# Kernel optimization log

Hardware: AMD Instinct MI355X
Metric: run time of the kernel (lower is better)

Reference implementation:

```python
import jax, jax.numpy as jnp
import numpy as np


def setup_inputs() -> dict:
    key = jax.random.key(0)
    k1, k2, k3 = jax.random.split(key, 3)
    B, S, D = 4, 2048, 1024   # batch, seq_len, hidden
    M = 65536                 # external memory size
    x = jax.random.normal(k1, (B, S, D), dtype=jnp.float32)
    keys = jax.random.normal(k2, (M, D), dtype=jnp.float32)
    vals = jax.random.normal(k3, (M, D), dtype=jnp.float32)
    return {"x": x, "ver": 1, "keys": keys, "vals": vals}


def reference(x, ver, keys, vals):
    # linear_attention: unnormalized attention over external memory.
    #   out = (x @ keys^T) @ vals
    # Use associativity to avoid materializing the [B,S,M] score matrix:
    #   kv = keys^T @ vals  -> [D, D]
    kv = jnp.einsum("md,me->de", keys, vals)   # [D, D]
    out = jnp.einsum("bsd,de->bse", x, kv)      # [B, S, D]
    return out
```

## Files before the change

kernel.cpp:

```cpp
#include <hip/hip_runtime.h>
#include <hip/hip_bf16.h>


typedef __attribute__((ext_vector_type(8))) __bf16 bf16x8;
typedef __attribute__((ext_vector_type(4))) __bf16 bf16x4;
typedef __attribute__((ext_vector_type(4))) float  f32x4;

#define D_DIM   1024
#define M_DIM   65536
#define ROWS    8192
#define NCHUNK  16
#define MC      (M_DIM / NCHUNK)
#define BT      128
#define BK      64
#define LDK     72
#define TILE_BYTES 16384

__device__ __forceinline__ f32x4 mfma16(bf16x8 a, bf16x8 b, f32x4 c) {
    return __builtin_amdgcn_mfma_f32_16x16x32_bf16(a, b, c, 0, 0, 0);
}

__device__ __forceinline__ void gl_lds16(const void* gsrc, void* ldst) {
    __builtin_amdgcn_global_load_lds(
        (const __attribute__((address_space(1))) unsigned int*)gsrc,
        (__attribute__((address_space(3))) unsigned int*)ldst,
        16, 0, 0);
}

__global__ __launch_bounds__(512)
void convert_tile(const float* __restrict__ keys,
                  const float* __restrict__ vals,
                  __hip_bfloat16* __restrict__ KtT,
                  __hip_bfloat16* __restrict__ VtT)
{
    __shared__ __align__(16) char Lt[1024 * 128];

    const float* src = blockIdx.z ? vals : keys;
    char* dstb = (char*)(blockIdx.z ? VtT : KtT);

    const int tid = threadIdx.x;
    const int s   = blockIdx.x;
    const int m0  = s * 64;

    const int dc = tid & 255;
    const int qh = tid >> 8;
    #pragma unroll
    for (int i = 0; i < 8; ++i) {
        const int q = 2 * i + qh;
        f32x4 v[4];
        #pragma unroll
        for (int r = 0; r < 4; ++r)
            v[r] = *(const f32x4*)(src + (size_t)(m0 + 4 * q + r) * D_DIM + 4 * dc);
        const int p8 = q ^ (dc & 15);
        #pragma unroll
        for (int j = 0; j < 4; ++j) {
            bf16x4 w;
            #pragma unroll
            for (int r = 0; r < 4; ++r) w[r] = (__bf16)v[r][j];
            *(bf16x4*)(Lt + (4 * dc + j) * 128 + p8 * 8) = w;
        }
    }
    __syncthreads();

    #pragma unroll
    for (int ii = 0; ii < 16; ++ii) {
        const int idx = tid + ii * 512;
        const int t   = idx >> 10;
        const int dl  = (idx >> 3) & 127;
        const int c   = idx & 7;
        const int d   = t * 128 + dl;
        const int cl  = c ^ (dl & 7);
        const int h   = (dl >> 2) & 15;
        const int g0  = (2 * cl)     ^ h;
        const int g1  = (2 * cl + 1) ^ h;
        bf16x4 lo = *(const bf16x4*)(Lt + d * 128 + g0 * 8);
        bf16x4 hi = *(const bf16x4*)(Lt + d * 128 + g1 * 8);
        bf16x8 w;
        w[0] = lo[0]; w[1] = lo[1]; w[2] = lo[2]; w[3] = lo[3];
        w[4] = hi[0]; w[5] = hi[1]; w[6] = hi[2]; w[7] = hi[3];
        char* dst_tile = dstb + ((size_t)t * 1024 + s) * TILE_BYTES;
        *(bf16x8*)(dst_tile + dl * 128 + c * 16) = w;
    }
}

__global__ __launch_bounds__(512, 2)
void kv_gemm8(const __hip_bfloat16* __restrict__ VtT,
              const __hip_bfloat16* __restrict__ KtT,
              float* __restrict__ kvw)
{
    __shared__ __align__(16) char lds[2][4][TILE_BYTES];

    const int tid  = threadIdx.x;
    const int lane = tid & 63;
    const int wave = tid >> 6;
    const int we   = wave >> 2;
    const int wd   = wave & 3;

    const int bx    = blockIdx.x;
    const int xcd   = bx & 7;
    const int idx   = bx >> 3;
    const int chunk = ((idx >> 4) << 3) | xcd;
    const int t16   = idx & 15;
    const int E8    = t16 >> 2;
    const int D8    = t16 & 3;

    const size_t step0 = (size_t)chunk * 64;

    const char* Vb = (const char*)VtT;
    const char* Kb = (const char*)KtT;

    const int l15 = lane & 15;
    const int l7  = lane & 7;
    const int hi  = lane >> 4;

    f32x4 acc[8][4] = {};

    auto tileptr = [&](const char* base, int rt, int t) -> const char* {
        return base + ((size_t)rt * 1024 + step0 + (size_t)t) * TILE_BYTES;
    };
    auto stage_sub = [&](int buf, int sub, const char* tile) {
        char* dst = &lds[buf][sub][wave * 1024];
        const char* s = tile + wave * 1024 + lane * 16;
        gl_lds16(s,        dst);
        gl_lds16(s + 8192, dst + 8192);
    };

    stage_sub(0, 0, tileptr(Vb, 2 * E8,     0));
    stage_sub(0, 1, tileptr(Vb, 2 * E8 + 1, 0));
    stage_sub(0, 2, tileptr(Kb, 2 * D8,     0));
    stage_sub(0, 3, tileptr(Kb, 2 * D8 + 1, 0));
    asm volatile("s_waitcnt vmcnt(0)" ::: "memory");
    __builtin_amdgcn_s_barrier();

    bf16x8 bfr[4][2];

    #pragma unroll 2
    for (int t = 0; t < 64; ++t) {
        const int buf = t & 1;
        const char* abase = &lds[buf][we][0];
        const char* bbase = &lds[buf][2 + (wd >> 1)][0];
        const int brow0 = (wd & 1) * 64;

        #pragma unroll
        for (int p = 0; p < 4; ++p) {
            bf16x8 afr[2][2];
            #pragma unroll
            for (int j = 0; j < 2; ++j)
                #pragma unroll
                for (int ks = 0; ks < 2; ++ks) {
                    const int row = (2 * p + j) * 16 + l15;
                    afr[j][ks] = *(const bf16x8*)(abase + row * 128
                                   + (((ks << 2) + hi) ^ l7) * 16);
                }
            if (p == 0) {
                #pragma unroll
                for (int n = 0; n < 4; ++n)
                    #pragma unroll
                    for (int ks = 0; ks < 2; ++ks) {
                        const int row = brow0 + n * 16 + l15;
                        bfr[n][ks] = *(const bf16x8*)(bbase + row * 128
                                       + (((ks << 2) + hi) ^ l7) * 16);
                    }
            }
            if (p == 0 && t + 1 < 64) {
                stage_sub(buf ^ 1, 0, tileptr(Vb, 2 * E8,     t + 1));
                stage_sub(buf ^ 1, 1, tileptr(Vb, 2 * E8 + 1, t + 1));
            }
            if (p == 1 && t + 1 < 64) {
                stage_sub(buf ^ 1, 2, tileptr(Kb, 2 * D8,     t + 1));
                stage_sub(buf ^ 1, 3, tileptr(Kb, 2 * D8 + 1, t + 1));
            }
            __builtin_amdgcn_s_barrier();
            asm volatile("s_waitcnt lgkmcnt(0)" ::: "memory");
            __builtin_amdgcn_sched_barrier(0);
            __builtin_amdgcn_s_setprio(1);
            #pragma unroll
            for (int j = 0; j < 2; ++j)
                #pragma unroll
                for (int n = 0; n < 4; ++n)
                    #pragma unroll
                    for (int ks = 0; ks < 2; ++ks)
                        acc[2 * p + j][n] = mfma16(afr[j][ks], bfr[n][ks],
                                                   acc[2 * p + j][n]);
            __builtin_amdgcn_s_setprio(0);
            if (p == 3)
                asm volatile("s_waitcnt vmcnt(0)" ::: "memory");
            __builtin_amdgcn_s_barrier();
        }
    }

    const int rb = hi * 4;
    #pragma unroll
    for (int mi = 0; mi < 8; ++mi) {
        #pragma unroll
        for (int ni = 0; ni < 4; ++ni) {
            const int d = D8 * 256 + wd * 64 + ni * 16 + l15;
            #pragma unroll
            for (int r = 0; r < 4; ++r) {
                const int e = E8 * 256 + we * 128 + mi * 16 + rb + r;
                atomicAdd(kvw + (size_t)e * D_DIM + d, acc[mi][ni][r]);
            }
        }
    }
}

__global__ __launch_bounds__(256)
void kv_partial_kernel(const float* __restrict__ keys,
                       const float* __restrict__ vals,
                       float* __restrict__ kvw)
{
    __shared__ __bf16 Ktl[BT][LDK];
    __shared__ __bf16 Vtl[BT][LDK];

    const int tid  = threadIdx.x;
    const int lane = tid & 63;
    const int wave = tid >> 6;
    const int wr   = wave >> 1;
    const int wc   = wave & 1;

    const int tile  = blockIdx.x & 63;
    const int chunk = blockIdx.x >> 6;
    const int d0 = (tile >> 3) * BT;
    const int e0 = (tile & 7) * BT;
    const size_t mbeg = (size_t)chunk * MC;

    f32x4 acc[4][4] = {};
    const int kg  = tid & 15;
    const int d4a = tid >> 4;

    for (int ms = 0; ms < MC; ms += BK) {
        #pragma unroll
        for (int i = 0; i < 2; ++i) {
            const int dloc = (d4a + i * 16) * 4;
            const size_t mrow = mbeg + ms + (size_t)kg * 4;
            f32x4 kr[4], vr[4];
            #pragma unroll
            for (int r = 0; r < 4; ++r) {
                kr[r] = *(const f32x4*)(keys + (mrow + r) * D_DIM + d0 + dloc);
                vr[r] = *(const f32x4*)(vals + (mrow + r) * D_DIM + e0 + dloc);
            }
            #pragma unroll
            for (int j = 0; j < 4; ++j) {
                bf16x4 wk, wv;
                #pragma unroll
                for (int r = 0; r < 4; ++r) {
                    wk[r] = (__bf16)kr[r][j];
                    wv[r] = (__bf16)vr[r][j];
                }
                *(bf16x4*)&Ktl[dloc + j][kg * 4] = wk;
                *(bf16x4*)&Vtl[dloc + j][kg * 4] = wv;
            }
        }
        __syncthreads();

        #pragma unroll
        for (int ks = 0; ks < BK; ks += 32) {
            bf16x8 af[4], bf[4];
            #pragma unroll
            for (int t = 0; t < 4; ++t) {
                af[t] = *(const bf16x8*)&Ktl[wr * 64 + t * 16 + (lane & 15)][ks + (lane >> 4) * 8];
                bf[t] = *(const bf16x8*)&Vtl[wc * 64 + t * 16 + (lane & 15)][ks + (lane >> 4) * 8];
            }
            #pragma unroll
            for (int mi = 0; mi < 4; ++mi)
                #pragma unroll
                for (int ni = 0; ni < 4; ++ni)
                    acc[mi][ni] = mfma16(af[mi], bf[ni], acc[mi][ni]);
        }
        __syncthreads();
    }

    const int rbase = (lane >> 4) * 4;
    const int cidx  = lane & 15;
    #pragma unroll
    for (int mi = 0; mi < 4; ++mi) {
        #pragma unroll
        for (int ni = 0; ni < 4; ++ni) {
            const int e = e0 + wc * 64 + ni * 16 + cidx;
            #pragma unroll
            for (int reg = 0; reg < 4; ++reg) {
                const int d = d0 + wr * 64 + mi * 16 + rbase + reg;
                atomicAdd(kvw + (size_t)e * D_DIM + d, acc[mi][ni][reg]);
            }
        }
    }
}

__global__ __launch_bounds__(256)
void out_gemm_kernel(const float* __restrict__ x,
                     const float* __restrict__ kvw,
                     float* __restrict__ out)
{
    __shared__ __bf16 Xt[BT][LDK];
    __shared__ __bf16 Wt[BT][LDK];

    const int tid  = threadIdx.x;
    const int lane = tid & 63;
    const int wave = tid >> 6;
    const int wr   = wave >> 1;
    const int wc   = wave & 1;

    const int r0 = blockIdx.x * BT;
    const int e0 = blockIdx.y * BT;

    f32x4 acc[4][4] = {};

    for (int ks0 = 0; ks0 < D_DIM; ks0 += BK) {
        #pragma unroll
        for (int i = 0; i < 8; ++i) {
            const int idx = tid + i * 256;
            const int row = idx >> 4;
            const int col = (idx & 15) * 4;
            f32x4 xa = *(const f32x4*)(x   + (size_t)(r0 + row) * D_DIM + ks0 + col);
            f32x4 wa = *(const f32x4*)(kvw + (size_t)(e0 + row) * D_DIM + ks0 + col);
            bf16x4 xb, wb;
            #pragma unroll
            for (int j = 0; j < 4; ++j) {
                xb[j] = (__bf16)xa[j];
                wb[j] = (__bf16)wa[j];
            }
            *(bf16x4*)&Xt[row][col] = xb;
            *(bf16x4*)&Wt[row][col] = wb;
        }
        __syncthreads();

        #pragma unroll
        for (int ks = 0; ks < BK; ks += 32) {
            bf16x8 af[4], bf[4];
            #pragma unroll
            for (int t = 0; t < 4; ++t) {
                af[t] = *(const bf16x8*)&Xt[wr * 64 + t * 16 + (lane & 15)][ks + (lane >> 4) * 8];
                bf[t] = *(const bf16x8*)&Wt[wc * 64 + t * 16 + (lane & 15)][ks + (lane >> 4) * 8];
            }
            #pragma unroll
            for (int mi = 0; mi < 4; ++mi)
                #pragma unroll
                for (int ni = 0; ni < 4; ++ni)
                    acc[mi][ni] = mfma16(af[mi], bf[ni], acc[mi][ni]);
        }
        __syncthreads();
    }

    const int rbase = (lane >> 4) * 4;
    const int cidx  = lane & 15;
    #pragma unroll
    for (int mi = 0; mi < 4; ++mi) {
        #pragma unroll
        for (int ni = 0; ni < 4; ++ni) {
            const int e = e0 + wc * 64 + ni * 16 + cidx;
            #pragma unroll
            for (int reg = 0; reg < 4; ++reg) {
                const int r = r0 + wr * 64 + mi * 16 + rbase + reg;
                out[(size_t)r * D_DIM + e] = acc[mi][ni][reg];
            }
        }
    }
}

extern "C" void kernel_launch(void* const* d_in, const int* in_sizes, int n_in,
                              void* d_out, int out_size, void* d_ws, size_t ws_size,
                              hipStream_t stream) {
    const float* x    = (const float*)d_in[0];
    const float* keys = (const float*)d_in[2];
    const float* vals = (const float*)d_in[3];
    float* out = (float*)d_out;

    const size_t kvw_bytes = (size_t)D_DIM * D_DIM * sizeof(float);
    const size_t kt_bytes  = (size_t)D_DIM * M_DIM * sizeof(__hip_bfloat16);
    const size_t need      = kvw_bytes + 2 * kt_bytes;

    float* kvw = (float*)d_ws;
    hipMemsetAsync(kvw, 0, kvw_bytes, stream);

    if (ws_size >= need) {
        __hip_bfloat16* KtT = (__hip_bfloat16*)((char*)d_ws + kvw_bytes);
        __hip_bfloat16* VtT = (__hip_bfloat16*)((char*)d_ws + kvw_bytes + kt_bytes);
        convert_tile<<<dim3(M_DIM / 64, 1, 2), dim3(512), 0, stream>>>(
            keys, vals, KtT, VtT);
        kv_gemm8<<<dim3(256), dim3(512), 0, stream>>>(VtT, KtT, kvw);
    } else {
        kv_partial_kernel<<<dim3(64 * NCHUNK), dim3(256), 0, stream>>>(keys, vals, kvw);
    }
    out_gemm_kernel<<<dim3(64, 8), dim3(256), 0, stream>>>(x, kvw, out);
}
```

Measured before the change: 353.9 us.

## Pre-convert x and kv to swizzled bf16 tiles for MFMA output GEMM

Adds a convert_rows kernel that turns x and the fp32 kv matrix into swizzled bf16 tiles. It also adds an out_gemm8 kernel that runs the output GEMM with bf16 MFMA, direct global-to-LDS loads and double buffering, in place of the old out_gemm_kernel. Separately, convert_tile is split along the D dimension so each block uses half the LDS, which doubles the grid and should raise occupancy. The new path needs extra workspace for the bf16 copies and falls back to the old kernel when the workspace is too small. The extra conversion passes add memory traffic and launch overhead, and rounding x and kv to bf16 reduces precision of the output.

```diff
diff --git a/kernel.cpp b/kernel.cpp
--- a/kernel.cpp
+++ b/kernel.cpp
@@ -33,24 +33,26 @@
                   __hip_bfloat16* __restrict__ KtT,
                   __hip_bfloat16* __restrict__ VtT)
 {
-    __shared__ __align__(16) char Lt[1024 * 128];
+    __shared__ __align__(16) char Lt[512 * 128];
 
     const float* src = blockIdx.z ? vals : keys;
     char* dstb = (char*)(blockIdx.z ? VtT : KtT);
 
-    const int tid = threadIdx.x;
-    const int s   = blockIdx.x;
-    const int m0  = s * 64;
-
-    const int dc = tid & 255;
-    const int qh = tid >> 8;
-    #pragma unroll
-    for (int i = 0; i < 8; ++i) {
-        const int q = 2 * i + qh;
+    const int tid  = threadIdx.x;
+    const int s    = blockIdx.x;
+    const int half = blockIdx.y;
+    const int m0   = s * 64;
+    const int d0   = half * 512;
+
+    const int dc = tid & 127;
+    const int qh = tid >> 7;
+    #pragma unroll
+    for (int i = 0; i < 4; ++i) {
+        const int q = 4 * i + qh;
         f32x4 v[4];
         #pragma unroll
         for (int r = 0; r < 4; ++r)
-            v[r] = *(const f32x4*)(src + (size_t)(m0 + 4 * q + r) * D_DIM + 4 * dc);
+            v[r] = *(const f32x4*)(src + (size_t)(m0 + 4 * q + r) * D_DIM + d0 + 4 * dc);
         const int p8 = q ^ (dc & 15);
         #pragma unroll
         for (int j = 0; j < 4; ++j) {
@@ -63,7 +65,7 @@
     __syncthreads();
 
     #pragma unroll
-    for (int ii = 0; ii < 16; ++ii) {
+    for (int ii = 0; ii < 8; ++ii) {
         const int idx = tid + ii * 512;
         const int t   = idx >> 10;
         const int dl  = (idx >> 3) & 127;
@@ -74,12 +76,36 @@
         const int g0  = (2 * cl)     ^ h;
         const int g1  = (2 * cl + 1) ^ h;
         bf16x4 lo = *(const bf16x4*)(Lt + d * 128 + g0 * 8);
-        bf16x4 hi = *(const bf16x4*)(Lt + d * 128 + g1 * 8);
+        bf16x4 hv = *(const bf16x4*)(Lt + d * 128 + g1 * 8);
         bf16x8 w;
         w[0] = lo[0]; w[1] = lo[1]; w[2] = lo[2]; w[3] = lo[3];
-        w[4] = hi[0]; w[5] = hi[1]; w[6] = hi[2]; w[7] = hi[3];
-        char* dst_tile = dstb + ((size_t)t * 1024 + s) * TILE_BYTES;
+        w[4] = hv[0]; w[5] = hv[1]; w[6] = hv[2]; w[7] = hv[3];
+        char* dst_tile = dstb + ((size_t)(half * 4 + t) * 1024 + s) * TILE_BYTES;
         *(bf16x8*)(dst_tile + dl * 128 + c * 16) = w;
+    }
+}
+
+__global__ __launch_bounds__(256)
+void convert_rows(const float* __restrict__ src,
+                  __hip_bfloat16* __restrict__ dstT)
+{
+    const int tid = threadIdx.x;
+    const int rt  = blockIdx.x;
+    const int t   = blockIdx.y;
+    const int r0  = rt * 128, d0 = t * 64;
+    char* tile = (char*)dstT + ((size_t)rt * 16 + t) * TILE_BYTES;
+    #pragma unroll
+    for (int it = 0; it < 4; ++it) {
+        const int idx = tid + it * 256;
+        const int r   = idx >> 3;
+        const int cl  = idx & 7;
+        const float* p = src + (size_t)(r0 + r) * D_DIM + d0 + cl * 8;
+        f32x4 a = *(const f32x4*)p;
+        f32x4 b = *(const f32x4*)(p + 4);
+        bf16x8 w;
+        w[0] = (__bf16)a[0]; w[1] = (__bf16)a[1]; w[2] = (__bf16)a[2]; w[3] = (__bf16)a[3];
+        w[4] = (__bf16)b[0]; w[5] = (__bf16)b[1]; w[6] = (__bf16)b[2]; w[7] = (__bf16)b[3];
+        *(bf16x8*)(tile + r * 128 + ((cl ^ (r & 7)) * 16)) = w;
     }
 }
 
@@ -204,6 +230,114 @@
     }
 }
 
+__global__ __launch_bounds__(512, 1)
+void out_gemm8(const __hip_bfloat16* __restrict__ xbT,
+               const __hip_bfloat16* __restrict__ kvbT,
+               float* __restrict__ out)
+{
+    __shared__ __align__(16) char lds[2][3][TILE_BYTES];
+
+    const int tid  = threadIdx.x;
+    const int lane = tid & 63;
+    const int wave = tid >> 6;
+    const int wr   = wave >> 2;
+    const int wee  = wave & 3;
+
+    const int bx = blockIdx.x;
+    const int rt = bx & 63;
+    const int be = bx >> 6;
+
+    const int l15 = lane & 15;
+    const int l7  = lane & 7;
+    const int hi  = lane >> 4;
+
+    f32x4 acc[4][4] = {};
+
+    const char* Xb = (const char*)xbT;
+    const char* Kv = (const char*)kvbT;
+
+    auto tileA = [&](int t) -> const char* {
+        return Xb + ((size_t)rt * 16 + t) * TILE_BYTES;
+    };
+    auto tileB = [&](int j, int t) -> const char* {
+        return Kv + ((size_t)(2 * be + j) * 16 + t) * TILE_BYTES;
+    };
+    auto stage_sub = [&](int buf, int sub, const char* tile) {
+        char* dst = &lds[buf][sub][wave * 1024];
+        const char* s = tile + wave * 1024 + lane * 16;
+        gl_lds16(s,        dst);
+        gl_lds16(s + 8192, dst + 8192);
+    };
+
+    stage_sub(0, 0, tileA(0));
+    stage_sub(0, 1, tileB(0, 0));
+    stage_sub(0, 2, tileB(1, 0));
+    asm volatile("s_waitcnt vmcnt(0)" ::: "memory");
+    __builtin_amdgcn_s_barrier();
+
+    bf16x8 bfr[4][2];
+
+    for (int t = 0; t < 16; ++t) {
+        const int buf = t & 1;
+        const char* abase = &lds[buf][0][0];
+        const char* bbase = &lds[buf][1 + (wee >> 1)][0];
+        const int brow0 = (wee & 1) * 64;
+
+        #pragma unroll
+        for (int p = 0; p < 4; ++p) {
+            bf16x8 afr[2];
+            #pragma unroll
+            for (int ks = 0; ks < 2; ++ks) {
+                const int row = wr * 64 + p * 16 + l15;
+                afr[ks] = *(const bf16x8*)(abase + row * 128
+                              + (((ks << 2) + hi) ^ l7) * 16);
+            }
+            if (p == 0) {
+                #pragma unroll
+                for (int n = 0; n < 4; ++n)
+                    #pragma unroll
+                    for (int ks = 0; ks < 2; ++ks) {
+                        const int row = brow0 + n * 16 + l15;
+                        bfr[n][ks] = *(const bf16x8*)(bbase + row * 128
+                                       + (((ks << 2) + hi) ^ l7) * 16);
+                    }
+            }
+            if (p == 0 && t + 1 < 16) stage_sub(buf ^ 1, 0, tileA(t + 1));
+            if (p == 1 && t + 1 < 16) {
+                stage_sub(buf ^ 1, 1, tileB(0, t + 1));
+                stage_sub(buf ^ 1, 2, tileB(1, t + 1));
+            }
+            __builtin_amdgcn_s_barrier();
+            asm volatile("s_waitcnt lgkmcnt(0)" ::: "memory");
+            __builtin_amdgcn_sched_barrier(0);
+            __builtin_amdgcn_s_setprio(1);
+            #pragma unroll
+            for (int n = 0; n < 4; ++n)
+                #pragma unroll
+                for (int ks = 0; ks < 2; ++ks)
+                    acc[p][n] = mfma16(afr[ks], bfr[n][ks], acc[p][n]);
+            __builtin_amdgcn_s_setprio(0);
+            if (p == 3)
+                asm volatile("s_waitcnt vmcnt(0)" ::: "memory");
+            __builtin_amdgcn_s_barrier();
+        }
+    }
+
+    const int r0 = rt * 128, e0 = be * 256;
+    #pragma unroll
+    for (int mi = 0; mi < 4; ++mi) {
+        #pragma unroll
+        for (int ni = 0; ni < 4; ++ni) {
+            const int e = e0 + wee * 64 + ni * 16 + l15;
+            #pragma unroll
+            for (int r = 0; r < 4; ++r) {
+                const int rr = r0 + wr * 64 + mi * 16 + hi * 4 + r;
+                out[(size_t)rr * D_DIM + e] = acc[mi][ni][r];
+            }
+        }
+    }
+}
+
 __global__ __launch_bounds__(256)
 void kv_partial_kernel(const float* __restrict__ keys,
                        const float* __restrict__ vals,
@@ -367,19 +501,32 @@
 
     const size_t kvw_bytes = (size_t)D_DIM * D_DIM * sizeof(float);
     const size_t kt_bytes  = (size_t)D_DIM * M_DIM * sizeof(__hip_bfloat16);
-    const size_t need      = kvw_bytes + 2 * kt_bytes;
+    const size_t xb_bytes  = (size_t)ROWS * D_DIM * sizeof(__hip_bfloat16);
+    const size_t kvb_bytes = (size_t)D_DIM * D_DIM * sizeof(__hip_bfloat16);
+    const size_t need_kv   = kvw_bytes + 2 * kt_bytes;
+    const size_t need_full = need_kv + xb_bytes + kvb_bytes;
 
     float* kvw = (float*)d_ws;
     hipMemsetAsync(kvw, 0, kvw_bytes, stream);
 
-    if (ws_size >= need) {
+    if (ws_size >= need_kv) {
         __hip_bfloat16* KtT = (__hip_bfloat16*)((char*)d_ws + kvw_bytes);
         __hip_bfloat16* VtT = (__hip_bfloat16*)((char*)d_ws + kvw_bytes + kt_bytes);
-        convert_tile<<<dim3(M_DIM / 64, 1, 2), dim3(512), 0, stream>>>(
+        convert_tile<<<dim3(M_DIM / 64, 2, 2), dim3(512), 0, stream>>>(
             keys, vals, KtT, VtT);
         kv_gemm8<<<dim3(256), dim3(512), 0, stream>>>(VtT, KtT, kvw);
+
+        if (ws_size >= need_full) {
+            __hip_bfloat16* xbT  = (__hip_bfloat16*)((char*)d_ws + need_kv);
+            __hip_bfloat16* kvbT = (__hip_bfloat16*)((char*)d_ws + need_kv + xb_bytes);
+            convert_rows<<<dim3(ROWS / 128, 16), dim3(256), 0, stream>>>(x, xbT);
+            convert_rows<<<dim3(D_DIM / 128, 16), dim3(256), 0, stream>>>(kvw, kvbT);
+            out_gemm8<<<dim3(256), dim3(512), 0, stream>>>(xbT, kvbT, out);
+        } else {
+            out_gemm_kernel<<<dim3(64, 8), dim3(256), 0, stream>>>(x, kvw, out);
+        }
     } else {
         kv_partial_kernel<<<dim3(64 * NCHUNK), dim3(256), 0, stream>>>(keys, vals, kvw);
-    }
-    out_gemm_kernel<<<dim3(64, 8), dim3(256), 0, stream>>>(x, kvw, out);
-}
+        out_gemm_kernel<<<dim3(64, 8), dim3(256), 0, stream>>>(x, kvw, out);
+    }
+}
```

After: 376.1 us. 6.3% more time.
